# Performance work log

Hardware: AMD Instinct MI355X
Metric: run time of the kernel (lower is better)

Reference implementation:

```python
import jax, jax.numpy as jnp
import numpy as np

N_QUBITS = 8
N_QLAYERS = 7
EPS = 1e-12


def _conv(x, w, b, stride, pad):
    y = jax.lax.conv_general_dilated(x, w, (stride, stride), [(pad, pad), (pad, pad)],
                                     dimension_numbers=("NCHW", "OIHW", "NCHW"))
    return y + b[None, :, None, None]


def _adaptive_avg_pool(x, out):
    # torch AdaptiveAvgPool2d semantics: bin i = [floor(i*H/out), ceil((i+1)*H/out))
    H, W = x.shape[-2], x.shape[-1]
    hs = [(i * H) // out for i in range(out)]
    he = [-(-((i + 1) * H) // out) for i in range(out)]
    ws = [(i * W) // out for i in range(out)]
    we = [-(-((i + 1) * W) // out) for i in range(out)]
    xh = jnp.stack([x[:, :, s:e, :].mean(axis=2) for s, e in zip(hs, he)], axis=2)
    return jnp.stack([xh[:, :, :, s:e].mean(axis=3) for s, e in zip(ws, we)], axis=3)


def _ry(st, theta, wire):
    # st: [B, 2, 2, ..., 2]; RY = [[cos, -sin], [sin, cos]] (real)
    c, s = jnp.cos(theta / 2), jnp.sin(theta / 2)
    U = jnp.stack([jnp.stack([c, -s]), jnp.stack([s, c])])  # [2,2]
    m = jnp.moveaxis(st, wire + 1, -1)
    m = m @ U.T
    return jnp.moveaxis(m, -1, wire + 1)


def _cnot(st, ctrl, tgt):
    s = jnp.moveaxis(st, (ctrl + 1, tgt + 1), (1, 2))
    s = jnp.stack([s[:, 0], jnp.flip(s[:, 1], axis=1)], axis=1)
    return jnp.moveaxis(s, (1, 2), (ctrl + 1, tgt + 1))


def _quantum(feat, q_w):
    B = feat.shape[0]
    psi = feat / jnp.maximum(jnp.linalg.norm(feat, axis=1, keepdims=True), EPS)
    st = psi.reshape((B,) + (2,) * N_QUBITS)  # wire 0 = most significant axis
    for l in range(N_QLAYERS):
        for q in range(N_QUBITS):
            st = _ry(st, q_w[l, q], q)
        for q in range(N_QUBITS - 1):
            st = _cnot(st, q, q + 1)
    s2 = st.reshape(B, 2, -1)
    return jnp.sum(s2[:, 0] ** 2, axis=-1) - jnp.sum(s2[:, 1] ** 2, axis=-1)  # [B]


def _forward(x, conv1_w, conv1_b, conv2_w, conv2_b, conv3_w, conv3_b, fc_w, fc_b, q_w,
             c1_w, c1_b, c2_w, c2_b, c3_w, c3_b, c4_w, c4_b, c5_w, c5_b):
    h = jax.nn.relu(_conv(x, conv1_w, conv1_b, 2, 2))   # [B,8,14,14]
    h = jax.nn.relu(_conv(h, conv2_w, conv2_b, 2, 1))   # [B,16,7,7]
    h = jax.nn.relu(_conv(h, conv3_w, conv3_b, 1, 1))   # [B,32,7,7]
    h = _adaptive_avg_pool(h, 3)                         # [B,32,3,3]
    h = h.reshape(h.shape[0], -1)                        # [B,288]
    feat = jax.nn.relu(h @ fc_w.T + fc_b)                # [B,256] (dropout = eval no-op)
    feat = feat / jnp.maximum(jnp.linalg.norm(feat, axis=1, keepdims=True), EPS)
    q = _quantum(feat, q_w)[:, None]                     # [B,1]
    h = jax.nn.relu(q @ c1_w.T + c1_b)
    h = jax.nn.relu(h @ c2_w.T + c2_b)
    h = jax.nn.relu(h @ c3_w.T + c3_b)
    h = jax.nn.relu(h @ c4_w.T + c4_b)
    return jax.nn.sigmoid(h @ c5_w.T + c5_b)             # [B,1]


def setup_inputs() -> dict:
    key = jax.random.key(0)
    ks = jax.random.split(key, 32)
    B = 8192
    def rn(k, shape, scale):
        return jax.random.normal(k, shape, dtype=jnp.float32) * scale
    return {
        "x": rn(ks[0], (B, 1, 28, 28), 1.0),
        "conv1_w": rn(ks[1], (8, 1, 5, 5), 0.2), "conv1_b": rn(ks[2], (8,), 0.05),
        "conv2_w": rn(ks[3], (16, 8, 3, 3), 0.12), "conv2_b": rn(ks[4], (16,), 0.05),
        "conv3_w": rn(ks[5], (32, 16, 3, 3), 0.08), "conv3_b": rn(ks[6], (32,), 0.05),
        "fc_w": rn(ks[7], (256, 288), 0.06), "fc_b": rn(ks[8], (256,), 0.02),
        "q_w": rn(ks[9], (7, 8), 1.0),
        "c1_w": rn(ks[10], (512, 1), 0.5), "c1_b": rn(ks[11], (512,), 0.02),
        "c2_w": rn(ks[12], (256, 512), 0.04), "c2_b": rn(ks[13], (256,), 0.02),
        "c3_w": rn(ks[14], (128, 256), 0.06), "c3_b": rn(ks[15], (128,), 0.02),
        "c4_w": rn(ks[16], (64, 128), 0.09), "c4_b": rn(ks[17], (64,), 0.02),
        "c5_w": rn(ks[18], (1, 64), 0.12), "c5_b": rn(ks[19], (1,), 0.02),
    }


def reference(x, conv1_w, conv1_b, conv2_w, conv2_b, conv3_w, conv3_b, fc_w, fc_b, q_w,
              c1_w, c1_b, c2_w, c2_b, c3_w, c3_b, c4_w, c4_b, c5_w, c5_b):
    return _forward(x, conv1_w, conv1_b, conv2_w, conv2_b, conv3_w, conv3_b, fc_w, fc_b, q_w,
                    c1_w, c1_b, c2_w, c2_b, c3_w, c3_b, c4_w, c4_b, c5_w, c5_b)
```

## Files before the change

### kernel.cpp

```cpp
#include <hip/hip_runtime.h>
#include <math.h>


__global__ __launch_bounds__(256) void k_conv12(
    const float* __restrict__ x,
    const float* __restrict__ w1, const float* __restrict__ b1,
    const float* __restrict__ w2, const float* __restrict__ b2,
    float* __restrict__ y2p) {
  __shared__ float xin[4][784];
  __shared__ float y1p[4][8][14][20];
  __shared__ float wl1[200], bl1[8];
  __shared__ float wl2t[72][16], bl2[16];
  const int n0 = blockIdx.x * 4;
  const int tid = threadIdx.x;

  for (int i = tid; i < 200; i += 256) wl1[i] = w1[i];
  if (tid < 8) bl1[tid] = b1[tid];
  for (int i = tid; i < 1152; i += 256) {
    int k = i >> 4, co = i & 15;
    wl2t[k][co] = w2[co * 72 + k];
  }
  if (tid < 16) bl2[tid] = b2[tid];
#pragma unroll
  for (int s = 0; s < 4; ++s)
    if (tid < 196)
      reinterpret_cast<float4*>(&xin[s][0])[tid] =
          reinterpret_cast<const float4*>(&x[(size_t)(n0 + s) * 784])[tid];
  __syncthreads();

  if (tid < 224) {
    const int s = tid / 56, r = tid % 56, co = r / 7, oyh = r % 7;
    float wreg[25];
#pragma unroll
    for (int i = 0; i < 25; ++i) wreg[i] = wl1[co * 25 + i];
    const float bb = bl1[co];
#pragma unroll
    for (int half = 0; half < 2; ++half) {
      const int oy = oyh + half * 7;
      float acc[14];
#pragma unroll
      for (int ox = 0; ox < 14; ++ox) acc[ox] = bb;
#pragma unroll
      for (int ky = 0; ky < 5; ++ky) {
        const int y = oy * 2 - 2 + ky;
        if (y >= 0 && y < 28) {
          const float4* xp = reinterpret_cast<const float4*>(&xin[s][y * 28]);
          float xr[28];
#pragma unroll
          for (int v = 0; v < 7; ++v) {
            float4 q = xp[v];
            xr[v * 4 + 0] = q.x; xr[v * 4 + 1] = q.y;
            xr[v * 4 + 2] = q.z; xr[v * 4 + 3] = q.w;
          }
#pragma unroll
          for (int kx = 0; kx < 5; ++kx) {
            const float w = wreg[ky * 5 + kx];
#pragma unroll
            for (int ox = 0; ox < 14; ++ox) {
              const int xx = ox * 2 - 2 + kx;
              if (xx >= 0 && xx < 28) acc[ox] += w * xr[xx];
            }
          }
        }
      }
#pragma unroll
      for (int ox = 0; ox < 14; ++ox) y1p[s][co][oy][ox] = fmaxf(acc[ox], 0.f);
    }
  }
  __syncthreads();

  if (tid < 224) {
    const int s = tid / 56, r = tid % 56, cop = r / 7, oy = r % 7;
    const int co0 = cop * 2;
    float acc0[7], acc1[7];
#pragma unroll
    for (int ox = 0; ox < 7; ++ox) { acc0[ox] = bl2[co0]; acc1[ox] = bl2[co0 + 1]; }
    for (int ci = 0; ci < 8; ++ci) {
#pragma unroll
      for (int ky = 0; ky < 3; ++ky) {
        const int y = oy * 2 - 1 + ky;
        if (y >= 0 && y < 14) {
          const float4* rp = reinterpret_cast<const float4*>(&y1p[s][ci][y][0]);
          float4 q0 = rp[0], q1 = rp[1], q2 = rp[2], q3 = rp[3];
          float xr[14] = {q0.x, q0.y, q0.z, q0.w, q1.x, q1.y, q1.z, q1.w,
                          q2.x, q2.y, q2.z, q2.w, q3.x, q3.y};
          const int kb = ci * 9 + ky * 3;
          const float wa0 = wl2t[kb + 0][co0],     wa1 = wl2t[kb + 1][co0],     wa2 = wl2t[kb + 2][co0];
          const float wb0 = wl2t[kb + 0][co0 + 1], wb1 = wl2t[kb + 1][co0 + 1], wb2 = wl2t[kb + 2][co0 + 1];
#pragma unroll
          for (int ox = 0; ox < 7; ++ox) {
            if (2 * ox - 1 >= 0) { acc0[ox] += wa0 * xr[2 * ox - 1]; acc1[ox] += wb0 * xr[2 * ox - 1]; }
            acc0[ox] += wa1 * xr[2 * ox];
            acc1[ox] += wb1 * xr[2 * ox];
            if (2 * ox + 1 < 14) { acc0[ox] += wa2 * xr[2 * ox + 1]; acc1[ox] += wb2 * xr[2 * ox + 1]; }
          }
        }
      }
    }
    float* o0 = &y2p[(size_t)(n0 + s) * 896 + (co0 + 0) * 56 + oy * 8];
    float* o1 = &y2p[(size_t)(n0 + s) * 896 + (co0 + 1) * 56 + oy * 8];
#pragma unroll
    for (int ox = 0; ox < 7; ++ox) {
      o0[ox] = fmaxf(acc0[ox], 0.f);
      o1[ox] = fmaxf(acc1[ox], 0.f);
    }
  }
}

__global__ __launch_bounds__(256) void k_conv3pool(
    const float* __restrict__ y2p,
    const float* __restrict__ w3, const float* __restrict__ b3,
    float* __restrict__ pooled) {
  __shared__ float y2s[8][16][7][8];
  __shared__ float wl3t[144][32];
  __shared__ float bl3[32];
  const int n0 = blockIdx.x * 8;
  const int tid = threadIdx.x;

  for (int i = tid; i < 4608; i += 256) {
    int k = i >> 5, co = i & 31;
    wl3t[k][co] = w3[co * 144 + k];
  }
  if (tid < 32) bl3[tid] = b3[tid];
#pragma unroll
  for (int s = 0; s < 8; ++s)
    if (tid < 224)
      reinterpret_cast<float4*>(&y2s[s][0][0][0])[tid] =
          reinterpret_cast<const float4*>(&y2p[(size_t)(n0 + s) * 896])[tid];
  __syncthreads();

  const int s = tid >> 5, co = tid & 31;
  float acc[49];
  {
    const float bb = bl3[co];
#pragma unroll
    for (int i = 0; i < 49; ++i) acc[i] = bb;
  }
  for (int ci = 0; ci < 16; ++ci) {
    float xr[7][7];
#pragma unroll
    for (int y = 0; y < 7; ++y) {
      const float4* rp = reinterpret_cast<const float4*>(&y2s[s][ci][y][0]);
      float4 qa = rp[0], qb = rp[1];
      xr[y][0] = qa.x; xr[y][1] = qa.y; xr[y][2] = qa.z; xr[y][3] = qa.w;
      xr[y][4] = qb.x; xr[y][5] = qb.y; xr[y][6] = qb.z;
    }
    float wreg[9];
#pragma unroll
    for (int k = 0; k < 9; ++k) wreg[k] = wl3t[ci * 9 + k][co];
#pragma unroll
    for (int ky = 0; ky < 3; ++ky)
#pragma unroll
      for (int kx = 0; kx < 3; ++kx) {
        const float w = wreg[ky * 3 + kx];
#pragma unroll
        for (int oy = 0; oy < 7; ++oy) {
          const int y = oy - 1 + ky;
          if (y >= 0 && y < 7) {
#pragma unroll
            for (int ox = 0; ox < 7; ++ox) {
              const int xx = ox - 1 + kx;
              if (xx >= 0 && xx < 7) acc[oy * 7 + ox] += w * xr[y][xx];
            }
          }
        }
      }
  }
#pragma unroll
  for (int i = 0; i < 49; ++i) acc[i] = fmaxf(acc[i], 0.f);
  float* out = pooled + (size_t)(n0 + s) * 288 + co * 9;
#pragma unroll
  for (int py = 0; py < 3; ++py)
#pragma unroll
    for (int px = 0; px < 3; ++px) {
      float v = 0.f;
#pragma unroll
      for (int dy = 0; dy < 3; ++dy)
#pragma unroll
        for (int dx = 0; dx < 3; ++dx) v += acc[(2 * py + dy) * 7 + (2 * px + dx)];
      out[py * 3 + px] = v * (1.f / 9.f);
    }
}

template <int NT, int EP, bool ASYNTH>
__global__ __launch_bounds__(256) void k_rowgemm16(
    const float* __restrict__ A, const float* __restrict__ Bm,
    const float* __restrict__ bias, float* __restrict__ C,
    const float* __restrict__ sq, const float* __restrict__ sw,
    const float* __restrict__ sb, int K) {
  static_assert(NT == 128 || NT == 256, "NT");
  constexpr int NC = NT / 128;
  constexpr int NB4 = NT / 32;
  constexpr int BS = NT + 4;
  __shared__ float AT[32 * 20];
  __shared__ float BT[32 * BS];
  const int m0 = blockIdx.x * 16;
  const int tid = threadIdx.x;
  const int tr = tid >> 5, tc = tid & 31;

  float ra[2];
  float4 rb[NB4];

  auto loadAB = [&](int k0) {
#pragma unroll
    for (int e = 0; e < 2; ++e) {
      const int idx = tid + e * 256;
      const int mm = idx >> 5, kk = idx & 31;
      if (ASYNTH) ra[e] = fmaxf(sq[m0 + mm] * sw[k0 + kk] + sb[k0 + kk], 0.f);
      else ra[e] = A[(size_t)(m0 + mm) * K + k0 + kk];
    }
#pragma unroll
    for (int e = 0; e < NB4; ++e) {
      const int idx4 = tid + e * 256;
      const int nn = idx4 >> 3, kq = idx4 & 7;
      rb[e] = *reinterpret_cast<const float4*>(&Bm[(size_t)nn * K + k0 + kq * 4]);
    }
  };
  auto storeAB = [&]() {
#pragma unroll
    for (int e = 0; e < 2; ++e) {
      const int idx = tid + e * 256;
      AT[(idx & 31) * 20 + (idx >> 5)] = ra[e];
    }
#pragma unroll
    for (int e = 0; e < NB4; ++e) {
      const int idx4 = tid + e * 256;
      const int nn = idx4 >> 3, kq = idx4 & 7;
      BT[(kq * 4 + 0) * BS + nn] = rb[e].x;
      BT[(kq * 4 + 1) * BS + nn] = rb[e].y;
      BT[(kq * 4 + 2) * BS + nn] = rb[e].z;
      BT[(kq * 4 + 3) * BS + nn] = rb[e].w;
    }
  };

  float acc[2][NC][4];
#pragma unroll
  for (int i = 0; i < 2; ++i)
#pragma unroll
    for (int nc = 0; nc < NC; ++nc)
#pragma unroll
      for (int j = 0; j < 4; ++j) acc[i][nc][j] = 0.f;

  loadAB(0);
  for (int k0 = 0; k0 < K; k0 += 32) {
    __syncthreads();
    storeAB();
    __syncthreads();
    if (k0 + 32 < K) loadAB(k0 + 32);
#pragma unroll
    for (int kk = 0; kk < 32; ++kk) {
      const float2 a2 = *reinterpret_cast<const float2*>(&AT[kk * 20 + tr * 2]);
#pragma unroll
      for (int nc = 0; nc < NC; ++nc) {
        const float4 b4 = *reinterpret_cast<const float4*>(
            &BT[kk * BS + nc * 128 + tc * 4]);
        acc[0][nc][0] += a2.x * b4.x; acc[0][nc][1] += a2.x * b4.y;
        acc[0][nc][2] += a2.x * b4.z; acc[0][nc][3] += a2.x * b4.w;
        acc[1][nc][0] += a2.y * b4.x; acc[1][nc][1] += a2.y * b4.y;
        acc[1][nc][2] += a2.y * b4.z; acc[1][nc][3] += a2.y * b4.w;
      }
    }
  }

  if (EP == 2) {
    float qp[2] = {0.f, 0.f};
#pragma unroll
    for (int i = 0; i < 2; ++i)
#pragma unroll
      for (int nc = 0; nc < NC; ++nc)
#pragma unroll
        for (int j = 0; j < 4; ++j) {
          const float v = acc[i][nc][j];
          qp[i] += (nc == 0) ? v * v : -v * v;
        }
#pragma unroll
    for (int i = 0; i < 2; ++i)
#pragma unroll
      for (int d = 1; d < 32; d <<= 1) qp[i] += __shfl_xor(qp[i], d, 64);
    if (tc == 0) {
#pragma unroll
      for (int i = 0; i < 2; ++i) C[m0 + tr * 2 + i] = qp[i];
    }
  } else if (EP == 1) {
    float t[2][NC][4];
    float ss[2] = {0.f, 0.f};
#pragma unroll
    for (int i = 0; i < 2; ++i)
#pragma unroll
      for (int nc = 0; nc < NC; ++nc)
#pragma unroll
        for (int j = 0; j < 4; ++j) {
          const float v = fmaxf(acc[i][nc][j] + bias[nc * 128 + tc * 4 + j], 0.f);
          t[i][nc][j] = v;
          ss[i] += v * v;
        }
#pragma unroll
    for (int i = 0; i < 2; ++i)
#pragma unroll
      for (int d = 1; d < 32; d <<= 1) ss[i] += __shfl_xor(ss[i], d, 64);
#pragma unroll
    for (int i = 0; i < 2; ++i) {
      const float sc = 1.f / fmaxf(sqrtf(ss[i]), 1e-12f);
#pragma unroll
      for (int nc = 0; nc < NC; ++nc) {
        float4 v;
        v.x = t[i][nc][0] * sc; v.y = t[i][nc][1] * sc;
        v.z = t[i][nc][2] * sc; v.w = t[i][nc][3] * sc;
        *reinterpret_cast<float4*>(&C[(size_t)(m0 + tr * 2 + i) * NT + nc * 128 + tc * 4]) = v;
      }
    }
  } else {
#pragma unroll
    for (int i = 0; i < 2; ++i)
#pragma unroll
      for (int nc = 0; nc < NC; ++nc) {
        float4 v;
        v.x = fmaxf(acc[i][nc][0] + bias[nc * 128 + tc * 4 + 0], 0.f);
        v.y = fmaxf(acc[i][nc][1] + bias[nc * 128 + tc * 4 + 1], 0.f);
        v.z = fmaxf(acc[i][nc][2] + bias[nc * 128 + tc * 4 + 2], 0.f);
        v.w = fmaxf(acc[i][nc][3] + bias[nc * 128 + tc * 4 + 3], 0.f);
        *reinterpret_cast<float4*>(&C[(size_t)(m0 + tr * 2 + i) * NT + nc * 128 + tc * 4]) = v;
      }
  }
}

template <int NT>
__global__ __launch_bounds__(256) void k_rowgemm64(
    const float* __restrict__ A, const float* __restrict__ Bm,
    const float* __restrict__ bias, float* __restrict__ C, int K) {
  constexpr int NB = NT / 64;
  __shared__ float AT[32 * 68];
  __shared__ float BT[32 * (NT + 4)];
  constexpr int BS = NT + 4;
  const int m0 = blockIdx.x * 64;
  const int tid = threadIdx.x;
  const int tr = tid >> 4, tc = tid & 15;
  float acc[4][NB][4];
#pragma unroll
  for (int i = 0; i < 4; ++i)
#pragma unroll
    for (int nb = 0; nb < NB; ++nb)
#pragma unroll
      for (int j = 0; j < 4; ++j) acc[i][nb][j] = 0.f;

  for (int k0 = 0; k0 < K; k0 += 32) {
#pragma unroll
    for (int e = 0; e < 8; ++e) {
      int idx = tid + e * 256;
      int mm = idx >> 5, kk = idx & 31;
      AT[kk * 68 + mm] = A[(size_t)(m0 + mm) * K + k0 + kk];
    }
#pragma unroll
    for (int e = 0; e < NB * 8; ++e) {
      int idx = tid + e * 256;
      int nn = idx >> 5, kk = idx & 31;
      BT[kk * BS + nn] = Bm[(size_t)nn * K + k0 + kk];
    }
    __syncthreads();
#pragma unroll
    for (int kk = 0; kk < 32; ++kk) {
      const float4 a4 = *reinterpret_cast<const float4*>(&AT[kk * 68 + tr * 4]);
      const float a[4] = {a4.x, a4.y, a4.z, a4.w};
#pragma unroll
      for (int nb = 0; nb < NB; ++nb) {
        const float4 b4 = *reinterpret_cast<const float4*>(&BT[kk * BS + nb * 64 + tc * 4]);
        const float b[4] = {b4.x, b4.y, b4.z, b4.w};
#pragma unroll
        for (int i = 0; i < 4; ++i)
#pragma unroll
          for (int j = 0; j < 4; ++j) acc[i][nb][j] += a[i] * b[j];
      }
    }
    __syncthreads();
  }
#pragma unroll
  for (int i = 0; i < 4; ++i)
#pragma unroll
    for (int nb = 0; nb < NB; ++nb) {
      float4 v;
      v.x = fmaxf(acc[i][nb][0] + bias[nb * 64 + tc * 4 + 0], 0.f);
      v.y = fmaxf(acc[i][nb][1] + bias[nb * 64 + tc * 4 + 1], 0.f);
      v.z = fmaxf(acc[i][nb][2] + bias[nb * 64 + tc * 4 + 2], 0.f);
      v.w = fmaxf(acc[i][nb][3] + bias[nb * 64 + tc * 4 + 3], 0.f);
      *reinterpret_cast<float4*>(&C[(size_t)(m0 + tr * 4 + i) * NT + nb * 64 + tc * 4]) = v;
    }
}

__global__ __launch_bounds__(64) void k_buildU(const float* __restrict__ qw,
                                               float* __restrict__ Uw) {
  const int j = blockIdx.x;
  const int t = threadIdx.x;
  float a0 = (t == j) ? 1.f : 0.f;
  float a1 = (64 + t == j) ? 1.f : 0.f;
  float a2 = (128 + t == j) ? 1.f : 0.f;
  float a3 = (192 + t == j) ? 1.f : 0.f;
  for (int l = 0; l < 7; ++l) {
#pragma unroll
    for (int q = 0; q < 8; ++q) {
      const float th = 0.5f * qw[l * 8 + q];
      const float c = cosf(th), s = sinf(th);
      const int m = 7 - q;
      if (m == 7) {
        const float n0 = c * a0 - s * a2, n2 = s * a0 + c * a2;
        const float n1 = c * a1 - s * a3, n3 = s * a1 + c * a3;
        a0 = n0; a2 = n2; a1 = n1; a3 = n3;
      } else if (m == 6) {
        const float n0 = c * a0 - s * a1, n1 = s * a0 + c * a1;
        const float n2 = c * a2 - s * a3, n3 = s * a2 + c * a3;
        a0 = n0; a1 = n1; a2 = n2; a3 = n3;
      } else {
        const float p0 = __shfl_xor(a0, 1 << m, 64);
        const float p1 = __shfl_xor(a1, 1 << m, 64);
        const float p2 = __shfl_xor(a2, 1 << m, 64);
        const float p3 = __shfl_xor(a3, 1 << m, 64);
        const float sgn = ((t >> m) & 1) ? s : -s;
        a0 = c * a0 + sgn * p0; a1 = c * a1 + sgn * p1;
        a2 = c * a2 + sgn * p2; a3 = c * a3 + sgn * p3;
      }
    }
#pragma unroll
    for (int q = 0; q < 7; ++q) {
      const int mc = 7 - q, mt = mc - 1;
      if (mc == 7) {
        const float tmp = a2; a2 = a3; a3 = tmp;
      } else if (mc == 6) {
        a1 = __shfl_xor(a1, 32, 64);
        a3 = __shfl_xor(a3, 32, 64);
      } else {
        const float p0 = __shfl_xor(a0, 1 << mt, 64);
        const float p1 = __shfl_xor(a1, 1 << mt, 64);
        const float p2 = __shfl_xor(a2, 1 << mt, 64);
        const float p3 = __shfl_xor(a3, 1 << mt, 64);
        if ((t >> mc) & 1) { a0 = p0; a1 = p1; a2 = p2; a3 = p3; }
      }
    }
  }
  Uw[(0 * 64 + t) * 256 + j] = a0;
  Uw[(1 * 64 + t) * 256 + j] = a1;
  Uw[(2 * 64 + t) * 256 + j] = a2;
  Uw[(3 * 64 + t) * 256 + j] = a3;
}

__global__ __launch_bounds__(256) void k_head5(const float* __restrict__ h4,
                                               const float* __restrict__ w,
                                               const float* __restrict__ b,
                                               float* __restrict__ out) {
  const int row = blockIdx.x * 4 + (threadIdx.x >> 6);
  const int lane = threadIdx.x & 63;
  float s = h4[(size_t)row * 64 + lane] * w[lane];
#pragma unroll
  for (int d = 32; d > 0; d >>= 1) s += __shfl_xor(s, d, 64);
  if (lane == 0) out[row] = 1.f / (1.f + expf(-(s + b[0])));
}

extern "C" void kernel_launch(void* const* d_in, const int* in_sizes, int n_in,
                              void* d_out, int out_size, void* d_ws, size_t ws_size,
                              hipStream_t stream) {
  const float* x       = (const float*)d_in[0];
  const float* conv1_w = (const float*)d_in[1];
  const float* conv1_b = (const float*)d_in[2];
  const float* conv2_w = (const float*)d_in[3];
  const float* conv2_b = (const float*)d_in[4];
  const float* conv3_w = (const float*)d_in[5];
  const float* conv3_b = (const float*)d_in[6];
  const float* fc_w    = (const float*)d_in[7];
  const float* fc_b    = (const float*)d_in[8];
  const float* q_w     = (const float*)d_in[9];
  const float* c1_w    = (const float*)d_in[10];
  const float* c1_b    = (const float*)d_in[11];
  const float* c2_w    = (const float*)d_in[12];
  const float* c2_b    = (const float*)d_in[13];
  const float* c3_w    = (const float*)d_in[14];
  const float* c3_b    = (const float*)d_in[15];
  const float* c4_w    = (const float*)d_in[16];
  const float* c4_b    = (const float*)d_in[17];
  const float* c5_w    = (const float*)d_in[18];
  const float* c5_b    = (const float*)d_in[19];
  float* out = (float*)d_out;
  char* ws = (char*)d_ws;

  float* y2p    = (float*)(ws + 0);
  float* pooled = (float*)(ws + 29360128);
  float* feat   = (float*)(ws + 0);
  float* Uw     = (float*)(ws + 8388608);
  float* qv     = (float*)(ws + 8650752);
  float* h2     = (float*)(ws + 8683520);
  float* h3     = (float*)(ws + 17072128);
  float* h4     = (float*)(ws + 21266432);
  (void)in_sizes; (void)n_in; (void)out_size; (void)ws_size;

  k_conv12<<<2048, 256, 0, stream>>>(x, conv1_w, conv1_b, conv2_w, conv2_b, y2p);
  k_conv3pool<<<1024, 256, 0, stream>>>(y2p, conv3_w, conv3_b, pooled);
  k_rowgemm16<256, 1, false><<<512, 256, 0, stream>>>(pooled, fc_w, fc_b, feat,
                                                      nullptr, nullptr, nullptr, 288);
  k_buildU<<<256, 64, 0, stream>>>(q_w, Uw);
  k_rowgemm16<256, 2, false><<<512, 256, 0, stream>>>(feat, Uw, nullptr, qv,
                                                      nullptr, nullptr, nullptr, 256);
  k_rowgemm16<256, 0, true><<<512, 256, 0, stream>>>(nullptr, c2_w, c2_b, h2,
                                                     qv, c1_w, c1_b, 512);
  k_rowgemm16<128, 0, false><<<512, 256, 0, stream>>>(h2, c3_w, c3_b, h3,
                                                      nullptr, nullptr, nullptr, 256);
  k_rowgemm64<64><<<128, 256, 0, stream>>>(h3, c4_w, c4_b, h4, 128);
  k_head5<<<2048, 256, 0, stream>>>(h4, c5_w, c5_b, out);
}
```

Before: 350.2 us.

## Use split-bf16 MFMA for quantum unitary and c2 GEMMs

Replaces the FP32 row-GEMM kernels for the quantum state application and the c2 layer with a new MFMA kernel that emulates FP32 through a three-product bf16 hi/lo split. The unitary builder now emits hi/lo bf16 halves, and a new pre-pass splits c2 weights the same way. The quantum GEMM also fuses the <Z0> squared-amplitude reduction into its epilogue. This trades exact FP32 for roughly FP32-level accuracy and adds an extra launch and workspace buffers for the weight splits.

```diff
diff --git a/kernel.cpp b/kernel.cpp
--- a/kernel.cpp
+++ b/kernel.cpp
@@ -1,6 +1,14 @@
 #include <hip/hip_runtime.h>
 #include <math.h>
 
+
+typedef __attribute__((ext_vector_type(8))) short bf16x8;
+typedef __attribute__((ext_vector_type(4))) float f32x4;
+
+__device__ __forceinline__ unsigned rne_bf16(float x) {
+  unsigned u = __float_as_uint(x);
+  return (u + 0x7FFFu + ((u >> 16) & 1u)) & 0xFFFF0000u;
+}
 
 __global__ __launch_bounds__(256) void k_conv12(
     const float* __restrict__ x,
@@ -386,8 +394,22 @@
     }
 }
 
+__global__ __launch_bounds__(256) void k_splitW(const float* __restrict__ W,
+                                                short* __restrict__ Wh,
+                                                short* __restrict__ Wl, int n) {
+  const int i = blockIdx.x * 256 + threadIdx.x;
+  if (i < n) {
+    const float x = W[i];
+    const unsigned hb = rne_bf16(x);
+    const float lo = x - __uint_as_float(hb);
+    Wh[i] = (short)(hb >> 16);
+    Wl[i] = (short)(rne_bf16(lo) >> 16);
+  }
+}
+
 __global__ __launch_bounds__(64) void k_buildU(const float* __restrict__ qw,
-                                               float* __restrict__ Uw) {
+                                               short* __restrict__ Uh,
+                                               short* __restrict__ Ul) {
   const int j = blockIdx.x;
   const int t = threadIdx.x;
   float a0 = (t == j) ? 1.f : 0.f;
@@ -435,10 +457,108 @@
       }
     }
   }
-  Uw[(0 * 64 + t) * 256 + j] = a0;
-  Uw[(1 * 64 + t) * 256 + j] = a1;
-  Uw[(2 * 64 + t) * 256 + j] = a2;
-  Uw[(3 * 64 + t) * 256 + j] = a3;
+  const float av[4] = {a0, a1, a2, a3};
+#pragma unroll
+  for (int r = 0; r < 4; ++r) {
+    const float x = av[r];
+    const unsigned hb = rne_bf16(x);
+    const float lo = x - __uint_as_float(hb);
+    Uh[(r * 64 + t) * 256 + j] = (short)(hb >> 16);
+    Ul[(r * 64 + t) * 256 + j] = (short)(rne_bf16(lo) >> 16);
+  }
+}
+
+template <int MODE>
+__global__ __launch_bounds__(256) void k_mfma16(
+    const float* __restrict__ Afp, const short* __restrict__ Bh,
+    const short* __restrict__ Bl, const float* __restrict__ bias,
+    float* __restrict__ Cout, const float* __restrict__ sq,
+    const float* __restrict__ sw, const float* __restrict__ sb, int K) {
+  __shared__ float red[4][16];
+  const int m0 = blockIdx.x * 16;
+  const int tid = threadIdx.x;
+  const int wave = tid >> 6, lane = tid & 63;
+  const int lrow = lane & 15, lgrp = lane >> 4;
+  const int n0 = wave * 64;
+
+  f32x4 acc[4];
+#pragma unroll
+  for (int nt = 0; nt < 4; ++nt) acc[nt] = (f32x4){0.f, 0.f, 0.f, 0.f};
+
+  float qm = 0.f;
+  if (MODE == 0) qm = sq[m0 + lrow];
+  const float* arow = (MODE == 1) ? (Afp + (size_t)(m0 + lrow) * K) : Afp;
+
+  for (int k0 = 0; k0 < K; k0 += 32) {
+    const int kb = k0 + lgrp * 8;
+    float a[8];
+    if (MODE == 0) {
+      const float4 w0 = *reinterpret_cast<const float4*>(&sw[kb]);
+      const float4 w1 = *reinterpret_cast<const float4*>(&sw[kb + 4]);
+      const float4 b0 = *reinterpret_cast<const float4*>(&sb[kb]);
+      const float4 b1 = *reinterpret_cast<const float4*>(&sb[kb + 4]);
+      a[0] = fmaxf(qm * w0.x + b0.x, 0.f); a[1] = fmaxf(qm * w0.y + b0.y, 0.f);
+      a[2] = fmaxf(qm * w0.z + b0.z, 0.f); a[3] = fmaxf(qm * w0.w + b0.w, 0.f);
+      a[4] = fmaxf(qm * w1.x + b1.x, 0.f); a[5] = fmaxf(qm * w1.y + b1.y, 0.f);
+      a[6] = fmaxf(qm * w1.z + b1.z, 0.f); a[7] = fmaxf(qm * w1.w + b1.w, 0.f);
+    } else {
+      const float4 a0v = *reinterpret_cast<const float4*>(&arow[kb]);
+      const float4 a1v = *reinterpret_cast<const float4*>(&arow[kb + 4]);
+      a[0] = a0v.x; a[1] = a0v.y; a[2] = a0v.z; a[3] = a0v.w;
+      a[4] = a1v.x; a[5] = a1v.y; a[6] = a1v.z; a[7] = a1v.w;
+    }
+    bf16x8 ah, al;
+#pragma unroll
+    for (int i = 0; i < 8; ++i) {
+      const unsigned hb = rne_bf16(a[i]);
+      const float lo = a[i] - __uint_as_float(hb);
+      ah[i] = (short)(hb >> 16);
+      al[i] = (short)(rne_bf16(lo) >> 16);
+    }
+#pragma unroll
+    for (int nt = 0; nt < 4; ++nt) {
+      const size_t boff = (size_t)(n0 + nt * 16 + lrow) * K + kb;
+      const bf16x8 bh = *reinterpret_cast<const bf16x8*>(&Bh[boff]);
+      const bf16x8 bl = *reinterpret_cast<const bf16x8*>(&Bl[boff]);
+      acc[nt] = __builtin_amdgcn_mfma_f32_16x16x32_bf16(ah, bh, acc[nt], 0, 0, 0);
+      acc[nt] = __builtin_amdgcn_mfma_f32_16x16x32_bf16(ah, bl, acc[nt], 0, 0, 0);
+      acc[nt] = __builtin_amdgcn_mfma_f32_16x16x32_bf16(al, bh, acc[nt], 0, 0, 0);
+    }
+  }
+
+  if (MODE == 0) {
+#pragma unroll
+    for (int nt = 0; nt < 4; ++nt) {
+      const int col = n0 + nt * 16 + lrow;
+      const float bb = bias[col];
+#pragma unroll
+      for (int j = 0; j < 4; ++j) {
+        const int row = m0 + lgrp * 4 + j;
+        Cout[(size_t)row * 256 + col] = fmaxf(acc[nt][j] + bb, 0.f);
+      }
+    }
+  } else {
+    float p[4] = {0.f, 0.f, 0.f, 0.f};
+#pragma unroll
+    for (int nt = 0; nt < 4; ++nt)
+#pragma unroll
+      for (int j = 0; j < 4; ++j) { const float v = acc[nt][j]; p[j] += v * v; }
+    if (wave >= 2) {
+#pragma unroll
+      for (int j = 0; j < 4; ++j) p[j] = -p[j];
+    }
+#pragma unroll
+    for (int d = 1; d < 16; d <<= 1)
+#pragma unroll
+      for (int j = 0; j < 4; ++j) p[j] += __shfl_xor(p[j], d, 64);
+    if (lrow == 0) {
+#pragma unroll
+      for (int j = 0; j < 4; ++j) red[wave][lgrp * 4 + j] = p[j];
+    }
+    __syncthreads();
+    if (tid < 16)
+      Cout[m0 + tid] = red[0][tid] + red[1][tid] + red[2][tid] + red[3][tid];
+  }
 }
 
 __global__ __launch_bounds__(256) void k_head5(const float* __restrict__ h4,
@@ -481,23 +601,28 @@
 
   float* y2p    = (float*)(ws + 0);
   float* pooled = (float*)(ws + 29360128);
+  short* c2h    = (short*)(ws + 38797312);
+  short* c2l    = (short*)(ws + 39059456);
   float* feat   = (float*)(ws + 0);
-  float* Uw     = (float*)(ws + 8388608);
+  short* Uh     = (short*)(ws + 8388608);
+  short* Ul     = (short*)(ws + 8519680);
   float* qv     = (float*)(ws + 8650752);
   float* h2     = (float*)(ws + 8683520);
   float* h3     = (float*)(ws + 17072128);
   float* h4     = (float*)(ws + 21266432);
   (void)in_sizes; (void)n_in; (void)out_size; (void)ws_size;
 
+  k_splitW<<<512, 256, 0, stream>>>(c2_w, c2h, c2l, 256 * 512);
+
   k_conv12<<<2048, 256, 0, stream>>>(x, conv1_w, conv1_b, conv2_w, conv2_b, y2p);
   k_conv3pool<<<1024, 256, 0, stream>>>(y2p, conv3_w, conv3_b, pooled);
   k_rowgemm16<256, 1, false><<<512, 256, 0, stream>>>(pooled, fc_w, fc_b, feat,
                                                       nullptr, nullptr, nullptr, 288);
-  k_buildU<<<256, 64, 0, stream>>>(q_w, Uw);
-  k_rowgemm16<256, 2, false><<<512, 256, 0, stream>>>(feat, Uw, nullptr, qv,
-                                                      nullptr, nullptr, nullptr, 256);
-  k_rowgemm16<256, 0, true><<<512, 256, 0, stream>>>(nullptr, c2_w, c2_b, h2,
-                                                     qv, c1_w, c1_b, 512);
+  k_buildU<<<256, 64, 0, stream>>>(q_w, Uh, Ul);
+  k_mfma16<1><<<512, 256, 0, stream>>>(feat, Uh, Ul, nullptr, qv,
+                                       nullptr, nullptr, nullptr, 256);
+  k_mfma16<0><<<512, 256, 0, stream>>>(nullptr, c2h, c2l, c2_b, h2,
+                                       qv, c1_w, c1_b, 512);
   k_rowgemm16<128, 0, false><<<512, 256, 0, stream>>>(h2, c3_w, c3_b, h3,
                                                       nullptr, nullptr, nullptr, 256);
   k_rowgemm64<64><<<128, 256, 0, stream>>>(h3, c4_w, c4_b, h4, 128);
```

After: 328.6 us. 1.07x faster.
